# Performance work log

Measured on AMD Instinct MI355X. Metric: run time of the kernel, lower is better.

Reference implementation:

```python
import jax, jax.numpy as jnp
import numpy as np
from jax import lax

NUM_HEADS = 8
RATIO_H = 2
RATIO_W = 2


def _layer_norm(x, gamma, beta, eps=1e-5):
    mean = jnp.mean(x, axis=-1, keepdims=True)
    var = jnp.var(x, axis=-1, keepdims=True)
    return (x - mean) * lax.rsqrt(var + eps) * gamma + beta


def setup_inputs() -> dict:
    key = jax.random.key(0)
    ks = jax.random.split(key, 6)
    B, N, C = 4, 4096, 512
    std = 0.02
    return {
        "x": jax.random.normal(ks[0], (B, N, C), jnp.float32),
        "w_qkv": jax.random.normal(ks[1], (3 * C, C), jnp.float32) * std,
        "w_ke": jax.random.normal(ks[2], (C, C, RATIO_H, RATIO_W), jnp.float32) * std,
        "w_ve": jax.random.normal(ks[3], (C, C, RATIO_H, RATIO_W), jnp.float32) * std,
        "gamma_k": jnp.ones((C // NUM_HEADS,), jnp.float32),
        "beta_k": jnp.zeros((C // NUM_HEADS,), jnp.float32),
        "gamma_v": jnp.ones((C // NUM_HEADS,), jnp.float32),
        "beta_v": jnp.zeros((C // NUM_HEADS,), jnp.float32),
        "w_proj": jax.random.normal(ks[4], (C, C), jnp.float32) * std,
        "b_proj": jnp.zeros((C,), jnp.float32),
    }


def reference(x, w_qkv, w_ke, w_ve, gamma_k, beta_k, gamma_v, beta_v, w_proj, b_proj):
    B, N, C = x.shape
    H = W = int(np.sqrt(N))
    h = NUM_HEADS
    hd = C // h
    s = RATIO_H * RATIO_W
    scale = hd ** -0.5

    # qkv projection (no bias): [B, N, 3C]
    qkv = jnp.einsum('bnc,dc->bnd', x, w_qkv)
    q, k, v = jnp.split(qkv, 3, axis=-1)

    # q -> [B, h, N, hd]
    q = q.reshape(B, N, h, hd).transpose(0, 2, 1, 3)

    # spatial reduction of k, v via strided conv (kernel == stride, no bias)
    def reduce_kv(t, w):
        img = t.transpose(0, 2, 1).reshape(B, C, H, W)
        red = lax.conv_general_dilated(
            img, w, window_strides=(RATIO_H, RATIO_W), padding='VALID',
            dimension_numbers=('NCHW', 'OIHW', 'NCHW'))  # [B, C, H/rh, W/rw]
        return red.reshape(B, C, N // s).transpose(0, 2, 1).reshape(
            B, N // s, h, hd).transpose(0, 2, 1, 3)  # [B, h, N/s, hd]

    k = _layer_norm(reduce_kv(k, w_ke), gamma_k, beta_k)
    v = _layer_norm(reduce_kv(v, w_ve), gamma_v, beta_v)

    # attention: [B, h, N, N/s]
    attn = jax.nn.softmax(jnp.einsum('bhqd,bhkd->bhqk', q, k) * scale, axis=-1)
    out = jnp.einsum('bhqk,bhkd->bhqd', attn, v)  # [B, h, N, hd]
    out = out.transpose(0, 2, 1, 3).reshape(B, N, C)
    return jnp.einsum('bnc,dc->bnd', out, w_proj) + b_proj
```

## Files before the change

### kernel.cpp

```cpp
#include <hip/hip_runtime.h>
#include <hip/hip_bf16.h>

#define DEVI static __device__ __forceinline__

typedef __attribute__((ext_vector_type(4))) float f32x4;
typedef __attribute__((ext_vector_type(8))) short bf16x8;
typedef __attribute__((ext_vector_type(4))) short s16x4;
typedef __attribute__((ext_vector_type(2))) unsigned int u32x2;

DEVI unsigned short f2bf(float f) {
    union { float f; unsigned u; } v; v.f = f;
    unsigned r = v.u + 0x7fffu + ((v.u >> 16) & 1u);
    return (unsigned short)(r >> 16);
}

DEVI void gload_lds16(const void* g, void* l) {
    __builtin_amdgcn_global_load_lds(
        (const __attribute__((address_space(1))) unsigned int*)(g),
        (__attribute__((address_space(3))) unsigned int*)(l), 16, 0, 0);
}

#define EXP2A(d, x) asm("v_exp_f32 %0, %1" : "=v"(d) : "v"(x))
#define CVTPK(d, a, b) asm("v_cvt_pk_bf16_f32 %0, %1, %2" : "=v"(d) : "v"(a), "v"(b))

__global__ __launch_bounds__(256) void prep_kernel(
    const float* __restrict__ x, const float* __restrict__ w_qkv,
    const float* __restrict__ w_proj, const float* __restrict__ w_ke,
    const float* __restrict__ w_ve,
    unsigned short* __restrict__ xb, unsigned short* __restrict__ wqkvb,
    unsigned short* __restrict__ wprojb, unsigned short* __restrict__ w2k,
    unsigned short* __restrict__ w2v)
{
    const int blk = blockIdx.x, t = threadIdx.x;
    if (blk < 9216) {
        const float* src; unsigned short* dst; int i;
        if (blk < 8192)      { src = x;      dst = xb;     i = (blk * 256 + t) * 4; }
        else if (blk < 8960) { src = w_qkv;  dst = wqkvb;  i = ((blk - 8192) * 256 + t) * 4; }
        else                 { src = w_proj; dst = wprojb; i = ((blk - 8960) * 256 + t) * 4; }
        const float4 v = *(const float4*)(src + i);
        ushort4 o; o.x = f2bf(v.x); o.y = f2bf(v.y); o.z = f2bf(v.z); o.w = f2bf(v.w);
        *(ushort4*)(dst + i) = o;
    } else {
        const int r = blk - 9216;
        const float* wsrc = (r < 1024) ? w_ke : w_ve;
        unsigned short* wdst = (r < 1024) ? w2k : w2v;
        const int i4 = (((r & 1023) * 256) + t) * 4;
        const int o = i4 >> 11, p = (i4 >> 9) & 3, c = i4 & 511;
        const float* s = wsrc + (o << 11) + (c << 2) + p;
        ushort4 ov; ov.x = f2bf(s[0]); ov.y = f2bf(s[4]); ov.z = f2bf(s[8]); ov.w = f2bf(s[12]);
        *(ushort4*)(wdst + i4) = ov;
    }
}

template<int OUT_BF16, int ADD_BIAS>
__global__ __launch_bounds__(256) void gemm_bt(
    const unsigned short* __restrict__ A,
    const unsigned short* __restrict__ B,
    void* __restrict__ Cp, const float* __restrict__ bias,
    int N, int K)
{
    __shared__ unsigned short As[128 * 64];
    __shared__ unsigned short Bs[128 * 64];
    const int t = threadIdx.x;
    const int lane = t & 63, w = t >> 6;
    const int wr = w >> 1, wc = w & 1;
    const int lr = lane & 15, lg = lane >> 4;
    const size_t rowBase = (size_t)blockIdx.y * 128;
    const size_t colBase = (size_t)blockIdx.x * 128;

    const unsigned short* gA[4]; const unsigned short* gB[4]; int du[4];
#pragma unroll
    for (int j = 0; j < 4; ++j) {
        const int u = t * 16 + j * 4096;
        const int row = u >> 7, colb = u & 127;
        const int csw = colb ^ ((row & 7) << 4);
        du[j] = u;
        gA[j] = A + (rowBase + row) * (size_t)K + (csw >> 1);
        gB[j] = B + (colBase + row) * (size_t)K + (csw >> 1);
    }
    const int sw = (lr & 7) << 4;

    f32x4 acc[4][4] = {};

    for (int k0 = 0; k0 < K; k0 += 64) {
#pragma unroll
        for (int j = 0; j < 4; ++j) {
            gload_lds16(gA[j] + k0, (char*)As + du[j]);
            gload_lds16(gB[j] + k0, (char*)Bs + du[j]);
        }
        __syncthreads();
#pragma unroll
        for (int s = 0; s < 2; ++s) {
            const int ro = (s * 64 + lg * 16) ^ sw;
            bf16x8 af[4], bfr[4];
#pragma unroll
            for (int a = 0; a < 4; ++a)
                af[a] = *(const bf16x8*)((char*)As + (wr * 64 + a * 16 + lr) * 128 + ro);
#pragma unroll
            for (int bn = 0; bn < 4; ++bn)
                bfr[bn] = *(const bf16x8*)((char*)Bs + (wc * 64 + bn * 16 + lr) * 128 + ro);
#pragma unroll
            for (int a = 0; a < 4; ++a)
#pragma unroll
                for (int bn = 0; bn < 4; ++bn)
                    acc[a][bn] = __builtin_amdgcn_mfma_f32_16x16x32_bf16(af[a], bfr[bn], acc[a][bn], 0, 0, 0);
        }
        __syncthreads();
    }

#pragma unroll
    for (int a = 0; a < 4; ++a) {
        const size_t row = rowBase + wr * 64 + a * 16 + lg * 4;
#pragma unroll
        for (int bn = 0; bn < 4; ++bn) {
            const size_t col = colBase + wc * 64 + bn * 16 + lr;
#pragma unroll
            for (int r = 0; r < 4; ++r) {
                const float v = acc[a][bn][r];
                if (OUT_BF16) {
                    ((unsigned short*)Cp)[(row + r) * (size_t)N + col] = f2bf(v);
                } else {
                    const float vb2 = ADD_BIAS ? (v + bias[col]) : v;
                    ((float*)Cp)[(row + r) * (size_t)N + col] = vb2;
                }
            }
        }
    }
}

__global__ __launch_bounds__(256) void gemm_red(
    const unsigned short* __restrict__ qkvb,
    const unsigned short* __restrict__ w2k,
    const unsigned short* __restrict__ w2v,
    float* __restrict__ kred)
{
    __shared__ unsigned short As[128 * 64];
    __shared__ unsigned short Bs[128 * 64];
    const int t = threadIdx.x;
    const int lane = t & 63, w = t >> 6;
    const int wr = w >> 1, wc = w & 1;
    const int lr = lane & 15, lg = lane >> 4;
    const int rowBase = blockIdx.y * 128;
    const int colBase = blockIdx.x * 128;
    const int ks = blockIdx.z;
    const int isV = rowBase >= 4096;
    const unsigned short* Bp = isV ? w2v : w2k;

    const char* gA[4]; const unsigned short* gB[4]; int du[4];
#pragma unroll
    for (int j = 0; j < 4; ++j) {
        const int u = t * 16 + j * 4096;
        const int row = u >> 7, colb = u & 127;
        const int csw = colb ^ ((row & 7) << 4);
        du[j] = u;
        const int bm = (rowBase + row) & 4095;
        const int b = bm >> 10, m = bm & 1023;
        const int pix = (m >> 5) * 128 + (m & 31) * 2;
        gA[j] = (const char*)qkvb + ((size_t)(b * 4096 + pix) * 1536 + (isV ? 1024 : 512)) * 2 + csw;
        gB[j] = Bp + (colBase + row) * (size_t)2048 + (csw >> 1);
    }
    const int sw = (lr & 7) << 4;

    f32x4 acc[4][4] = {};

    for (int kk = 0; kk < 16; ++kk) {
        const int k0 = ks * 1024 + kk * 64;
        const int p = k0 >> 9;
        const int pd = ((p & 1) ? 1 : 0) + ((p & 2) ? 64 : 0);
        const size_t aoff = (size_t)pd * 3072 + (size_t)(k0 & 511) * 2;
#pragma unroll
        for (int j = 0; j < 4; ++j) {
            gload_lds16(gA[j] + aoff, (char*)As + du[j]);
            gload_lds16(gB[j] + k0, (char*)Bs + du[j]);
        }
        __syncthreads();
#pragma unroll
        for (int s = 0; s < 2; ++s) {
            const int ro = (s * 64 + lg * 16) ^ sw;
            bf16x8 af[4], bfr[4];
#pragma unroll
            for (int a = 0; a < 4; ++a)
                af[a] = *(const bf16x8*)((char*)As + (wr * 64 + a * 16 + lr) * 128 + ro);
#pragma unroll
            for (int bn = 0; bn < 4; ++bn)
                bfr[bn] = *(const bf16x8*)((char*)Bs + (wc * 64 + bn * 16 + lr) * 128 + ro);
#pragma unroll
            for (int a = 0; a < 4; ++a)
#pragma unroll
                for (int bn = 0; bn < 4; ++bn)
                    acc[a][bn] = __builtin_amdgcn_mfma_f32_16x16x32_bf16(af[a], bfr[bn], acc[a][bn], 0, 0, 0);
        }
        __syncthreads();
    }

    float* outp = kred + (size_t)ks * 4194304;
#pragma unroll
    for (int a = 0; a < 4; ++a) {
        const size_t row = (size_t)rowBase + wr * 64 + a * 16 + lg * 4;
#pragma unroll
        for (int bn = 0; bn < 4; ++bn) {
            const size_t col = (size_t)colBase + wc * 64 + bn * 16 + lr;
#pragma unroll
            for (int r = 0; r < 4; ++r)
                outp[(row + r) * 512 + col] = acc[a][bn][r];
        }
    }
}

__global__ __launch_bounds__(256) void ln_kernel(
    const float* __restrict__ kredA, const float* __restrict__ kredB,
    const float* __restrict__ gk, const float* __restrict__ bk,
    const float* __restrict__ gv, const float* __restrict__ bv,
    unsigned short* __restrict__ outp)
{
    const int bm = blockIdx.x;
    const int sel = blockIdx.y;
    const size_t off = ((size_t)sel * 4096 + bm) * 512;
    const float* g = sel ? gv : gk;
    const float* be = sel ? bv : bk;
    const float QS = sel ? 1.0f : 0.18033688011112042f;
    unsigned short* o = outp + off;
    const int t = threadIdx.x;
    const float2 a = *(const float2*)(kredA + off + t * 2);
    const float2 b2 = *(const float2*)(kredB + off + t * 2);
    const float vx = a.x + b2.x, vy = a.y + b2.y;
    float s = vx + vy, s2 = vx * vx + vy * vy;
#pragma unroll
    for (int o2 = 1; o2 <= 16; o2 <<= 1) {
        s += __shfl_xor(s, o2);
        s2 += __shfl_xor(s2, o2);
    }
    const float mean = s * 0.015625f;
    const float var = s2 * 0.015625f - mean * mean;
    const float rstd = rsqrtf(var + 1e-5f);
    const int c = (t * 2) & 63;
    ushort2 ov;
    ov.x = f2bf(((vx - mean) * rstd * g[c] + be[c]) * QS);
    ov.y = f2bf(((vy - mean) * rstd * g[c + 1] + be[c + 1]) * QS);
    *(ushort2*)(o + t * 2) = ov;
}

__global__ __launch_bounds__(256) void transpose_v(
    const unsigned short* __restrict__ v_ln, unsigned short* __restrict__ v_t)
{
    __shared__ unsigned short tile[64][65];
    const int mb = blockIdx.x;
    const int cb = blockIdx.y;
    const int t = threadIdx.x;
#pragma unroll
    for (int i = 0; i < 16; ++i) {
        const int idx = i * 256 + t;
        const int r = idx >> 6, c = idx & 63;
        tile[r][c] = v_ln[(size_t)(mb * 64 + r) * 512 + cb * 64 + c];
    }
    __syncthreads();
    const int b = mb >> 4;
    const int mloc = (mb & 15) * 64;
#pragma unroll
    for (int i = 0; i < 16; ++i) {
        const int idx = i * 256 + t;
        const int c = idx >> 6, m = idx & 63;
        v_t[((size_t)(b * 512) + cb * 64 + c) * 1024 + mloc + m] = tile[m][c];
    }
}

__global__ __launch_bounds__(256) void attn_kernel(
    const unsigned short* __restrict__ qkvb,
    const unsigned short* __restrict__ k_ln,
    const unsigned short* __restrict__ v_t,
    unsigned short* __restrict__ attn_out)
{
    extern __shared__ char smem[];
    const int blk = ((blockIdx.x & 7) << 7) | (blockIdx.x >> 3);
    const int qc = blk & 31, h = (blk >> 5) & 7, b = blk >> 8;
    const int t = threadIdx.x, w = t >> 6, lane = t & 63;
    const int lr = lane & 15, lg = lane >> 4;
    const int qrow0 = qc * 128 + w * 32;

    const unsigned short* qpA = qkvb + (size_t)(b * 4096 + qrow0 + lr) * 1536 + h * 64 + lg * 8;
    const bf16x8 qa0 = *(const bf16x8*)(qpA);
    const bf16x8 qa1 = *(const bf16x8*)(qpA + 32);
    const bf16x8 qb0 = *(const bf16x8*)(qpA + 16 * 1536);
    const bf16x8 qb1 = *(const bf16x8*)(qpA + 16 * 1536 + 32);

    const char* kbase = (const char*)(k_ln + (size_t)b * 524288 + h * 64);
    const char* vbase = (const char*)(v_t + ((size_t)b * 512 + h * 64) * 1024);
    const int d0 = t * 16, d1 = 4096 + t * 16;
    const int r0 = d0 >> 7, cs0 = (d0 & 127) ^ ((r0 & 7) << 4);
    const int r1 = d1 >> 7, cs1 = (d1 & 127) ^ ((r1 & 7) << 4);
    const char* gK0 = kbase + r0 * 1024 + cs0;
    const char* gK1 = kbase + r1 * 1024 + cs1;
    const char* gV0 = vbase + r0 * 2048 + cs0;
    const char* gV1 = vbase + r1 * 2048 + cs1;

#define STAGE_KV(buf, kt) do { \
    gload_lds16(gK0 + (size_t)(kt) * 65536, smem + (buf) * 8192 + d0); \
    gload_lds16(gK1 + (size_t)(kt) * 65536, smem + (buf) * 8192 + d1); \
    gload_lds16(gV0 + (kt) * 128, smem + 16384 + (buf) * 8192 + d0); \
    gload_lds16(gV1 + (kt) * 128, smem + 16384 + (buf) * 8192 + d1); \
  } while (0)

    f32x4 accA[4] = {}, accB[4] = {};
    float psA = 0.f, psB = 0.f;

    STAGE_KV(0, 0);
    __syncthreads();

    char* Pw = smem + 32768 + w * 2048;
    const int sw = (lr & 7) << 4;
    const int off0 = lr * 128 + ((lg * 16) ^ sw);
    const int off1 = lr * 128 + ((64 + lg * 16) ^ sw);
    int pwo[4];
#pragma unroll
    for (int tt = 0; tt < 4; ++tt) pwo[tt] = lr * 128 + ((tt * 32 + lg * 8) ^ sw);

#pragma unroll 2
    for (int kt = 0; kt < 16; ++kt) {
        const int cur = kt & 1;
        if (kt < 15) STAGE_KV(cur ^ 1, kt + 1);
        const char* KsB = smem + cur * 8192;
        const char* VsB = smem + 16384 + cur * 8192;

        f32x4 sa[4], sb[4];
#pragma unroll
        for (int tt = 0; tt < 4; ++tt) {
            const bf16x8 kf0 = *(const bf16x8*)(KsB + tt * 2048 + off0);
            const bf16x8 kf1 = *(const bf16x8*)(KsB + tt * 2048 + off1);
            f32x4 za = {}, zb = {};
            za = __builtin_amdgcn_mfma_f32_16x16x32_bf16(kf0, qa0, za, 0, 0, 0);
            za = __builtin_amdgcn_mfma_f32_16x16x32_bf16(kf1, qa1, za, 0, 0, 0);
            zb = __builtin_amdgcn_mfma_f32_16x16x32_bf16(kf0, qb0, zb, 0, 0, 0);
            zb = __builtin_amdgcn_mfma_f32_16x16x32_bf16(kf1, qb1, zb, 0, 0, 0);
            sa[tt] = za; sb[tt] = zb;
        }

#pragma unroll
        for (int tt = 0; tt < 4; ++tt) {
            float e0, e1, e2, e3;
            EXP2A(e0, sa[tt][0]); EXP2A(e1, sa[tt][1]);
            EXP2A(e2, sa[tt][2]); EXP2A(e3, sa[tt][3]);
            psA += (e0 + e1) + (e2 + e3);
            unsigned c0, c1;
            CVTPK(c0, e0, e1); CVTPK(c1, e2, e3);
            union { u32x2 u; s16x4 s; } pk; pk.u.x = c0; pk.u.y = c1;
            *(s16x4*)(Pw + pwo[tt]) = pk.s;
        }
        asm volatile("" ::: "memory");
        const bf16x8 fa0 = *(const bf16x8*)(Pw + off0);
        const bf16x8 fa1 = *(const bf16x8*)(Pw + off1);
        asm volatile("" ::: "memory");

#pragma unroll
        for (int tt = 0; tt < 4; ++tt) {
            float e0, e1, e2, e3;
            EXP2A(e0, sb[tt][0]); EXP2A(e1, sb[tt][1]);
            EXP2A(e2, sb[tt][2]); EXP2A(e3, sb[tt][3]);
            psB += (e0 + e1) + (e2 + e3);
            unsigned c0, c1;
            CVTPK(c0, e0, e1); CVTPK(c1, e2, e3);
            union { u32x2 u; s16x4 s; } pk; pk.u.x = c0; pk.u.y = c1;
            *(s16x4*)(Pw + pwo[tt]) = pk.s;
        }
        asm volatile("" ::: "memory");
        const bf16x8 fb0 = *(const bf16x8*)(Pw + off0);
        const bf16x8 fb1 = *(const bf16x8*)(Pw + off1);

#pragma unroll
        for (int n2 = 0; n2 < 4; ++n2) {
            const bf16x8 vf0 = *(const bf16x8*)(VsB + n2 * 2048 + off0);
            const bf16x8 vf1 = *(const bf16x8*)(VsB + n2 * 2048 + off1);
            accA[n2] = __builtin_amdgcn_mfma_f32_16x16x32_bf16(fa0, vf0, accA[n2], 0, 0, 0);
            accA[n2] = __builtin_amdgcn_mfma_f32_16x16x32_bf16(fa1, vf1, accA[n2], 0, 0, 0);
            accB[n2] = __builtin_amdgcn_mfma_f32_16x16x32_bf16(fb0, vf0, accB[n2], 0, 0, 0);
            accB[n2] = __builtin_amdgcn_mfma_f32_16x16x32_bf16(fb1, vf1, accB[n2], 0, 0, 0);
        }
        __syncthreads();
    }
#undef STAGE_KV

    psA += __shfl_xor(psA, 16); psA += __shfl_xor(psA, 32);
    psB += __shfl_xor(psB, 16); psB += __shfl_xor(psB, 32);
    const float invA = 1.0f / psA;
    const float invB = 1.0f / psB;
    float dA[4], dB[4];
#pragma unroll
    for (int r = 0; r < 4; ++r) {
        dA[r] = __shfl(invA, lg * 4 + r);
        dB[r] = __shfl(invB, lg * 4 + r);
    }
    unsigned short* oA = attn_out + (size_t)(b * 4096 + qrow0 + lg * 4) * 512 + h * 64;
#pragma unroll
    for (int n2 = 0; n2 < 4; ++n2)
#pragma unroll
        for (int r = 0; r < 4; ++r) {
            oA[(size_t)r * 512 + n2 * 16 + lr] = f2bf(accA[n2][r] * dA[r]);
            oA[(size_t)(16 + r) * 512 + n2 * 16 + lr] = f2bf(accB[n2][r] * dB[r]);
        }
}

extern "C" void kernel_launch(void* const* d_in, const int* in_sizes, int n_in,
                              void* d_out, int out_size, void* d_ws, size_t ws_size,
                              hipStream_t stream)
{
    (void)in_sizes; (void)n_in; (void)out_size; (void)ws_size;
    const float* x       = (const float*)d_in[0];
    const float* w_qkv   = (const float*)d_in[1];
    const float* w_ke    = (const float*)d_in[2];
    const float* w_ve    = (const float*)d_in[3];
    const float* gamma_k = (const float*)d_in[4];
    const float* beta_k  = (const float*)d_in[5];
    const float* gamma_v = (const float*)d_in[6];
    const float* beta_v  = (const float*)d_in[7];
    const float* w_proj  = (const float*)d_in[8];
    const float* b_proj  = (const float*)d_in[9];
    float* out = (float*)d_out;

    char* ws = (char*)d_ws;
    unsigned short* qkvb   = (unsigned short*)(ws + 0);
    unsigned short* xb     = (unsigned short*)(ws + 50331648);
    unsigned short* attn_o = xb;
    float*          kredB  = (float*)(ws + 67108864);
    float*          kredA  = (float*)(ws + 83886080);
    unsigned short* k_ln   = (unsigned short*)(ws + 100663296);
    unsigned short* v_ln   = (unsigned short*)(ws + 104857600);
    unsigned short* v_t    = (unsigned short*)(ws + 109051904);
    unsigned short* wqkvb  = (unsigned short*)(ws + 113246208);
    unsigned short* w2k    = (unsigned short*)(ws + 114819072);
    unsigned short* w2v    = (unsigned short*)(ws + 116916224);
    unsigned short* wprojb = (unsigned short*)(ws + 119013376);

    prep_kernel<<<11264, 256, 0, stream>>>(x, w_qkv, w_proj, w_ke, w_ve,
                                           xb, wqkvb, wprojb, w2k, w2v);

    gemm_bt<1, 0><<<dim3(12, 128), 256, 0, stream>>>(
        xb, wqkvb, qkvb, nullptr, 1536, 512);

    gemm_red<<<dim3(4, 64, 2), 256, 0, stream>>>(qkvb, w2k, w2v, kredB);

    ln_kernel<<<dim3(4096, 2), 256, 0, stream>>>(kredA, kredB,
                                                 gamma_k, beta_k, gamma_v, beta_v, k_ln);

    transpose_v<<<dim3(64, 8), 256, 0, stream>>>(v_ln, v_t);

    attn_kernel<<<1024, 256, 40960, stream>>>(qkvb, k_ln, v_t, attn_o);

    gemm_bt<0, 1><<<dim3(4, 128), 256, 0, stream>>>(
        attn_o, wprojb, out, b_proj, 512, 512);
}
```

Baseline: 161.2 us.

## Fold K/V projection weights into reduction conv weights, skip K/V projection

Precomputes combined weights (conv weight times the K or V slice of w_qkv) with a small new GEMM, so the strided reduction GEMM reads x directly instead of the projected K/V. The QKV projection now only produces Q (512 columns instead of 1536), and the attention kernel reads Q from a narrower buffer. This removes most of the large projection GEMM and its 48MB-class intermediate writes. The cost is an extra weight transpose and a small weight GEMM, plus one more bf16 rounding of the fused weights.

```diff
diff --git a/kernel.cpp b/kernel.cpp
--- a/kernel.cpp
+++ b/kernel.cpp
@@ -29,7 +29,7 @@
     const float* __restrict__ w_ve,
     unsigned short* __restrict__ xb, unsigned short* __restrict__ wqkvb,
     unsigned short* __restrict__ wprojb, unsigned short* __restrict__ w2k,
-    unsigned short* __restrict__ w2v)
+    unsigned short* __restrict__ w2v, unsigned short* __restrict__ wqkvT)
 {
     const int blk = blockIdx.x, t = threadIdx.x;
     if (blk < 9216) {
@@ -40,7 +40,7 @@
         const float4 v = *(const float4*)(src + i);
         ushort4 o; o.x = f2bf(v.x); o.y = f2bf(v.y); o.z = f2bf(v.z); o.w = f2bf(v.w);
         *(ushort4*)(dst + i) = o;
-    } else {
+    } else if (blk < 11264) {
         const int r = blk - 9216;
         const float* wsrc = (r < 1024) ? w_ke : w_ve;
         unsigned short* wdst = (r < 1024) ? w2k : w2v;
@@ -49,6 +49,15 @@
         const float* s = wsrc + (o << 11) + (c << 2) + p;
         ushort4 ov; ov.x = f2bf(s[0]); ov.y = f2bf(s[4]); ov.z = f2bf(s[8]); ov.w = f2bf(s[12]);
         *(ushort4*)(wdst + i4) = ov;
+    } else {
+        const int r2 = blk - 11264;
+        const int i4 = (r2 * 256 + t) * 4;
+        const int sel = i4 >> 18;
+        const int rem = i4 & 262143;
+        const int d = rem >> 9, c4 = rem & 511;
+        const float* s = w_qkv + (size_t)(512 + sel * 512 + c4) * 512 + d;
+        ushort4 ov; ov.x = f2bf(s[0]); ov.y = f2bf(s[512]); ov.z = f2bf(s[1024]); ov.w = f2bf(s[1536]);
+        *(ushort4*)(wqkvT + i4) = ov;
     }
 }
 
@@ -128,10 +137,83 @@
     }
 }
 
-__global__ __launch_bounds__(256) void gemm_red(
-    const unsigned short* __restrict__ qkvb,
+__global__ __launch_bounds__(256) void gemm_wt(
     const unsigned short* __restrict__ w2k,
     const unsigned short* __restrict__ w2v,
+    const unsigned short* __restrict__ wqkvT,
+    unsigned short* __restrict__ wtk,
+    unsigned short* __restrict__ wtv)
+{
+    __shared__ unsigned short As[128 * 64];
+    __shared__ unsigned short Bs[128 * 64];
+    const int t = threadIdx.x;
+    const int lane = t & 63, w = t >> 6;
+    const int wr = w >> 1, wc = w & 1;
+    const int lr = lane & 15, lg = lane >> 4;
+    const int rowBase = blockIdx.y * 128;
+    const int colBase = blockIdx.x * 128;
+    const int p = blockIdx.z & 3, sel = blockIdx.z >> 2;
+    const unsigned short* A = (sel ? w2v : w2k) + p * 512;
+    const unsigned short* B = wqkvT + (size_t)sel * 262144;
+    unsigned short* C = (sel ? wtv : wtk) + p * 512;
+
+    const unsigned short* gA[4]; const unsigned short* gB[4]; int du[4];
+#pragma unroll
+    for (int j = 0; j < 4; ++j) {
+        const int u = t * 16 + j * 4096;
+        const int row = u >> 7, colb = u & 127;
+        const int csw = colb ^ ((row & 7) << 4);
+        du[j] = u;
+        gA[j] = A + (size_t)(rowBase + row) * 2048 + (csw >> 1);
+        gB[j] = B + (size_t)(colBase + row) * 512 + (csw >> 1);
+    }
+    const int sw = (lr & 7) << 4;
+
+    f32x4 acc[4][4] = {};
+
+    for (int k0 = 0; k0 < 512; k0 += 64) {
+#pragma unroll
+        for (int j = 0; j < 4; ++j) {
+            gload_lds16(gA[j] + k0, (char*)As + du[j]);
+            gload_lds16(gB[j] + k0, (char*)Bs + du[j]);
+        }
+        __syncthreads();
+#pragma unroll
+        for (int s = 0; s < 2; ++s) {
+            const int ro = (s * 64 + lg * 16) ^ sw;
+            bf16x8 af[4], bfr[4];
+#pragma unroll
+            for (int a = 0; a < 4; ++a)
+                af[a] = *(const bf16x8*)((char*)As + (wr * 64 + a * 16 + lr) * 128 + ro);
+#pragma unroll
+            for (int bn = 0; bn < 4; ++bn)
+                bfr[bn] = *(const bf16x8*)((char*)Bs + (wc * 64 + bn * 16 + lr) * 128 + ro);
+#pragma unroll
+            for (int a = 0; a < 4; ++a)
+#pragma unroll
+                for (int bn = 0; bn < 4; ++bn)
+                    acc[a][bn] = __builtin_amdgcn_mfma_f32_16x16x32_bf16(af[a], bfr[bn], acc[a][bn], 0, 0, 0);
+        }
+        __syncthreads();
+    }
+
+#pragma unroll
+    for (int a = 0; a < 4; ++a) {
+        const size_t row = (size_t)rowBase + wr * 64 + a * 16 + lg * 4;
+#pragma unroll
+        for (int bn = 0; bn < 4; ++bn) {
+            const size_t col = (size_t)colBase + wc * 64 + bn * 16 + lr;
+#pragma unroll
+            for (int r = 0; r < 4; ++r)
+                C[(row + r) * 2048 + col] = f2bf(acc[a][bn][r]);
+        }
+    }
+}
+
+__global__ __launch_bounds__(256) void gemm_red(
+    const unsigned short* __restrict__ xb,
+    const unsigned short* __restrict__ wtk,
+    const unsigned short* __restrict__ wtv,
     float* __restrict__ kred)
 {
     __shared__ unsigned short As[128 * 64];
@@ -144,7 +226,7 @@
     const int colBase = blockIdx.x * 128;
     const int ks = blockIdx.z;
     const int isV = rowBase >= 4096;
-    const unsigned short* Bp = isV ? w2v : w2k;
+    const unsigned short* Bp = isV ? wtv : wtk;
 
     const char* gA[4]; const unsigned short* gB[4]; int du[4];
 #pragma unroll
@@ -156,7 +238,7 @@
         const int bm = (rowBase + row) & 4095;
         const int b = bm >> 10, m = bm & 1023;
         const int pix = (m >> 5) * 128 + (m & 31) * 2;
-        gA[j] = (const char*)qkvb + ((size_t)(b * 4096 + pix) * 1536 + (isV ? 1024 : 512)) * 2 + csw;
+        gA[j] = (const char*)xb + (size_t)(b * 4096 + pix) * 1024 + csw;
         gB[j] = Bp + (colBase + row) * (size_t)2048 + (csw >> 1);
     }
     const int sw = (lr & 7) << 4;
@@ -167,7 +249,7 @@
         const int k0 = ks * 1024 + kk * 64;
         const int p = k0 >> 9;
         const int pd = ((p & 1) ? 1 : 0) + ((p & 2) ? 64 : 0);
-        const size_t aoff = (size_t)pd * 3072 + (size_t)(k0 & 511) * 2;
+        const size_t aoff = (size_t)pd * 1024 + (size_t)(k0 & 511) * 2;
 #pragma unroll
         for (int j = 0; j < 4; ++j) {
             gload_lds16(gA[j] + aoff, (char*)As + du[j]);
@@ -265,7 +347,7 @@
 }
 
 __global__ __launch_bounds__(256) void attn_kernel(
-    const unsigned short* __restrict__ qkvb,
+    const unsigned short* __restrict__ qb,
     const unsigned short* __restrict__ k_ln,
     const unsigned short* __restrict__ v_t,
     unsigned short* __restrict__ attn_out)
@@ -277,11 +359,11 @@
     const int lr = lane & 15, lg = lane >> 4;
     const int qrow0 = qc * 128 + w * 32;
 
-    const unsigned short* qpA = qkvb + (size_t)(b * 4096 + qrow0 + lr) * 1536 + h * 64 + lg * 8;
+    const unsigned short* qpA = qb + (size_t)(b * 4096 + qrow0 + lr) * 512 + h * 64 + lg * 8;
     const bf16x8 qa0 = *(const bf16x8*)(qpA);
     const bf16x8 qa1 = *(const bf16x8*)(qpA + 32);
-    const bf16x8 qb0 = *(const bf16x8*)(qpA + 16 * 1536);
-    const bf16x8 qb1 = *(const bf16x8*)(qpA + 16 * 1536 + 32);
+    const bf16x8 qb0 = *(const bf16x8*)(qpA + 16 * 512);
+    const bf16x8 qb1 = *(const bf16x8*)(qpA + 16 * 512 + 32);
 
     const char* kbase = (const char*)(k_ln + (size_t)b * 524288 + h * 64);
     const char* vbase = (const char*)(v_t + ((size_t)b * 512 + h * 64) * 1024);
@@ -416,7 +498,10 @@
     float* out = (float*)d_out;
 
     char* ws = (char*)d_ws;
-    unsigned short* qkvb   = (unsigned short*)(ws + 0);
+    unsigned short* qb     = (unsigned short*)(ws + 0);
+    unsigned short* wtk    = (unsigned short*)(ws + 16777216);
+    unsigned short* wtv    = (unsigned short*)(ws + 18874368);
+    unsigned short* wqkvT  = (unsigned short*)(ws + 20971520);
     unsigned short* xb     = (unsigned short*)(ws + 50331648);
     unsigned short* attn_o = xb;
     float*          kredB  = (float*)(ws + 67108864);
@@ -429,20 +514,22 @@
     unsigned short* w2v    = (unsigned short*)(ws + 116916224);
     unsigned short* wprojb = (unsigned short*)(ws + 119013376);
 
-    prep_kernel<<<11264, 256, 0, stream>>>(x, w_qkv, w_proj, w_ke, w_ve,
-                                           xb, wqkvb, wprojb, w2k, w2v);
-
-    gemm_bt<1, 0><<<dim3(12, 128), 256, 0, stream>>>(
-        xb, wqkvb, qkvb, nullptr, 1536, 512);
-
-    gemm_red<<<dim3(4, 64, 2), 256, 0, stream>>>(qkvb, w2k, w2v, kredB);
+    prep_kernel<<<11776, 256, 0, stream>>>(x, w_qkv, w_proj, w_ke, w_ve,
+                                           xb, wqkvb, wprojb, w2k, w2v, wqkvT);
+
+    gemm_wt<<<dim3(4, 4, 8), 256, 0, stream>>>(w2k, w2v, wqkvT, wtk, wtv);
+
+    gemm_bt<1, 0><<<dim3(4, 128), 256, 0, stream>>>(
+        xb, wqkvb, qb, nullptr, 512, 512);
+
+    gemm_red<<<dim3(4, 64, 2), 256, 0, stream>>>(xb, wtk, wtv, kredB);
 
     ln_kernel<<<dim3(4096, 2), 256, 0, stream>>>(kredA, kredB,
                                                  gamma_k, beta_k, gamma_v, beta_v, k_ln);
 
     transpose_v<<<dim3(64, 8), 256, 0, stream>>>(v_ln, v_t);
 
-    attn_kernel<<<1024, 256, 40960, stream>>>(qkvb, k_ln, v_t, attn_o);
+    attn_kernel<<<1024, 256, 40960, stream>>>(qb, k_ln, v_t, attn_o);
 
     gemm_bt<0, 1><<<dim3(4, 128), 256, 0, stream>>>(
         attn_o, wprojb, out, b_proj, 512, 512);
```

After: 147.8 us. 8.3% less time.
